# Performance work log

Measured on AMD Instinct MI355X. Metric: run time of the kernel, lower is better.

The kernel has to match this reference:

```python
import jax, jax.numpy as jnp
import numpy as np

NUM_NODES = 2048
NUM_REL = 8
HIDDEN = 256


def setup_inputs() -> dict:
    key = jax.random.key(0)
    k1, k2, k3 = jax.random.split(key, 3)
    X = jax.random.normal(k1, (NUM_NODES, HIDDEN, NUM_REL), dtype=jnp.float32)
    A = jax.random.uniform(k2, (NUM_NODES, NUM_NODES, NUM_REL), dtype=jnp.float32)
    # nn.init.normal_(std=0.01)
    weight = 0.01 * jax.random.normal(k3, (HIDDEN, HIDDEN, NUM_REL), dtype=jnp.float32)
    return {"X": X, "A": A, "weight": weight}


def _tensor_product(A, B):
    # Faithful to the original: FFT along last (relation) dim, take REAL part of
    # both transformed operands, per-slice matmul, then real part of ifft.
    Af = jnp.real(jnp.fft.fft(A, axis=-1))  # (n1, n2, k)
    Bf = jnp.real(jnp.fft.fft(B, axis=-1))  # (n2, n4, k)
    C = jnp.einsum('nmk,mhk->nhk', Af, Bf)  # batched real matmul over slices k
    return jnp.real(jnp.fft.ifft(C, axis=-1)).astype(A.dtype)


def reference(X, A, weight):
    res = _tensor_product(A, X)          # (num_nodes, hidden, num_rel)
    res = _tensor_product(res, weight)   # (num_nodes, hidden, num_rel)
    return res
```

## Files before the change

kernel.cpp:

```cpp
#include <hip/hip_runtime.h>


typedef __bf16 bf16_t;
typedef __bf16 bf16x2 __attribute__((ext_vector_type(2)));
typedef __bf16 bf16x8 __attribute__((ext_vector_type(8)));
typedef float f32x4 __attribute__((ext_vector_type(4)));

#define R2C 0.70710678118654752f

__device__ __forceinline__ size_t swz(int r, int c, int K) {
  return (size_t)r * K + (c & ~63) + ((((c >> 3) & 7) ^ (r & 7)) << 3) + (c & 7);
}

__device__ __forceinline__ void async_cp16(const void* g, void* l) {
  __builtin_amdgcn_global_load_lds((const __attribute__((address_space(1))) char*)g,
                                   (__attribute__((address_space(3))) char*)l,
                                   16, 0, 0);
}

__device__ __forceinline__ void fwd5(const float x[8], float F[5]) {
  float s04 = x[0] + x[4], d04 = x[0] - x[4];
  float s26 = x[2] + x[6];
  float s15 = x[1] + x[5], s37 = x[3] + x[7];
  float t = (x[1] + x[7]) - (x[3] + x[5]);
  float e = s04 + s26, o = s15 + s37;
  F[0] = e + o;
  F[1] = d04 + R2C * t;
  F[2] = s04 - s26;
  F[3] = d04 - R2C * t;
  F[4] = e - o;
}

__global__ __launch_bounds__(256) void k_pre(const float* __restrict__ X,
                                             const float* __restrict__ A,
                                             const float* __restrict__ W,
                                             bf16_t* __restrict__ Xft,
                                             bf16_t* __restrict__ Af,
                                             bf16_t* __restrict__ Wft) {
  __shared__ bf16_t tx[40][256];
  int b = blockIdx.x;
  if (b < 8192) {
    size_t t = (size_t)b * 256 + threadIdx.x;
    size_t idx = t * 2;
    int n = (int)(idx >> 11), m = (int)(idx & 2047);
    const float4* p = (const float4*)(A + idx * 8);
    float4 q0 = p[0], q1 = p[1], q2 = p[2], q3 = p[3];
    float x0[8] = {q0.x, q0.y, q0.z, q0.w, q1.x, q1.y, q1.z, q1.w};
    float x1[8] = {q2.x, q2.y, q2.z, q2.w, q3.x, q3.y, q3.z, q3.w};
    float F0[5], F1[5];
    fwd5(x0, F0);
    fwd5(x1, F1);
    size_t pos = swz(n, m, 2048);
#pragma unroll
    for (int j = 0; j < 5; j++) {
      bf16x2 v = {(bf16_t)F0[j], (bf16_t)F1[j]};
      *(bf16x2*)(Af + (size_t)j * 4194304 + pos) = v;
    }
  } else if (b < 8448) {
    int bx = b - 8192;
    int m0 = (bx & 7) * 256, h0 = (bx >> 3) * 8;
    int t = threadIdx.x;
    const float4* p = (const float4*)(X + (((size_t)(m0 + t) * 256) + h0) * 8);
#pragma unroll
    for (int h = 0; h < 8; h++) {
      float4 a = p[2 * h], bb = p[2 * h + 1];
      float x[8] = {a.x, a.y, a.z, a.w, bb.x, bb.y, bb.z, bb.w};
      float F[5];
      fwd5(x, F);
#pragma unroll
      for (int j = 0; j < 5; j++) tx[j * 8 + h][t] = (bf16_t)F[j];
    }
    __syncthreads();
#pragma unroll
    for (int it = 0; it < 5; it++) {
      int slot = it * 256 + t;
      int row = slot >> 5, ch = slot & 31;
      int j = row >> 3, hl = row & 7;
      int h = h0 + hl;
      size_t gpos = (size_t)j * 524288 + (size_t)h * 2048 + m0 +
                    ((ch & ~7) << 3) + (((ch & 7) ^ (h & 7)) << 3);
      *(uint4*)(Xft + gpos) = *(const uint4*)(&tx[row][ch * 8]);
    }
  } else {
    int h = b - 8448;
    int hp = threadIdx.x;
    const float4* p = (const float4*)(W + ((size_t)hp * 256 + h) * 8);
    float4 a = p[0], bb = p[1];
    float x[8] = {a.x, a.y, a.z, a.w, bb.x, bb.y, bb.z, bb.w};
    float F[5];
    fwd5(x, F);
    const float sc[5] = {0.125f, 0.25f, 0.25f, 0.25f, 0.125f};
    size_t pos = swz(h, hp, 256);
#pragma unroll
    for (int j = 0; j < 5; j++)
      Wft[(size_t)j * 65536 + pos] = (bf16_t)(F[j] * sc[j]);
  }
}

__global__ __launch_bounds__(256) void gemm_ring(const bf16_t* __restrict__ A,
                                                 const bf16_t* __restrict__ B,
                                                 bf16_t* __restrict__ C, int K,
                                                 size_t ap, size_t bp, size_t cp) {
  __shared__ bf16_t sm[65536];
  const int j = blockIdx.z;
  const bf16_t* Aj = A + (size_t)j * ap;
  const bf16_t* Bj = B + (size_t)j * bp;
  bf16_t* Cj = C + (size_t)j * cp;
  const int n0 = blockIdx.x * 128, h0 = blockIdx.y * 128;
  const int tid = threadIdx.x;
  const int wv = tid >> 6, ln = tid & 63;
  const int quad = ln >> 4, l16 = ln & 15;
  const int wn = (wv & 1) * 64, wh = (wv >> 1) * 64;

  const bf16_t* ga[4];
  const bf16_t* gb[4];
  int lo[4];
#pragma unroll
  for (int s = 0; s < 4; s++) {
    int slot = s * 256 + tid;
    int row = slot >> 3, c16 = slot & 7;
    ga[s] = Aj + (size_t)(n0 + row) * K + c16 * 8;
    gb[s] = Bj + (size_t)(h0 + row) * K + c16 * 8;
    lo[s] = (s * 256 + wv * 64) * 8;
  }

  const int T = K >> 6;
#pragma unroll
  for (int i = 0; i < 3; i++) {
#pragma unroll
    for (int s = 0; s < 4; s++) {
      async_cp16(ga[s] + i * 64, sm + i * 8192 + lo[s]);
      async_cp16(gb[s] + i * 64, sm + 32768 + i * 8192 + lo[s]);
    }
  }

  f32x4 acc[4][4] = {};
  for (int t = 0; t < T; t++) {
    int b = t & 3;
    if (t + 3 < T) {
      int nb = (t + 3) & 3;
#pragma unroll
      for (int s = 0; s < 4; s++) {
        async_cp16(ga[s] + (t + 3) * 64, sm + nb * 8192 + lo[s]);
        async_cp16(gb[s] + (t + 3) * 64, sm + 32768 + nb * 8192 + lo[s]);
      }
      __builtin_amdgcn_s_waitcnt(0x4F78);
    } else if (t + 2 < T) {
      __builtin_amdgcn_s_waitcnt(0x4F70);
    } else if (t + 1 < T) {
      __builtin_amdgcn_s_waitcnt(0xF78);
    } else {
      __builtin_amdgcn_s_waitcnt(0xF70);
    }
    __builtin_amdgcn_s_barrier();
    const bf16_t* Asp = sm + b * 8192;
    const bf16_t* Bsp = sm + 32768 + b * 8192;
#pragma unroll
    for (int kh = 0; kh < 2; kh++) {
      bf16x8 af[4], bfr[4];
      int c16 = kh * 4 + quad;
#pragma unroll
      for (int i = 0; i < 4; i++) {
        int ra = wn + i * 16 + l16;
        int rb = wh + i * 16 + l16;
        af[i] = *(const bf16x8*)(Asp + ra * 64 + ((c16 ^ (ra & 7)) << 3));
        bfr[i] = *(const bf16x8*)(Bsp + rb * 64 + ((c16 ^ (rb & 7)) << 3));
      }
#pragma unroll
      for (int i = 0; i < 4; i++)
#pragma unroll
        for (int t2 = 0; t2 < 4; t2++)
          acc[i][t2] = __builtin_amdgcn_mfma_f32_16x16x32_bf16(af[i], bfr[t2],
                                                               acc[i][t2], 0, 0, 0);
    }
    __builtin_amdgcn_s_barrier();
  }
#pragma unroll
  for (int i = 0; i < 4; i++) {
#pragma unroll
    for (int t = 0; t < 4; t++) {
      int hc = h0 + wh + t * 16 + l16;
#pragma unroll
      for (int rg = 0; rg < 4; rg++) {
        int nr = n0 + wn + i * 16 + quad * 4 + rg;
        Cj[swz(nr, hc, 256)] = (bf16_t)acc[i][t][rg];
      }
    }
  }
}

__global__ __launch_bounds__(256) void gemm_flat(const bf16_t* __restrict__ A,
                                                 const bf16_t* __restrict__ B,
                                                 float* __restrict__ C) {
  __shared__ bf16_t sm[65536];
  const int j = blockIdx.z;
  const bf16_t* Aj = A + (size_t)j * 524288;
  const bf16_t* Bj = B + (size_t)j * 65536;
  float* Cj = C + (size_t)j * 524288;
  const int n0 = blockIdx.x * 128, h0 = blockIdx.y * 128;
  const int tid = threadIdx.x;
  const int wv = tid >> 6, ln = tid & 63;
  const int quad = ln >> 4, l16 = ln & 15;
  const int wn = (wv & 1) * 64, wh = (wv >> 1) * 64;

#pragma unroll
  for (int s = 0; s < 16; s++) {
    int st = s * 256 + tid;
    int row = st >> 5, c = st & 31;
    int lo = (s * 256 + wv * 64) * 8;
    async_cp16(Aj + (size_t)(n0 + row) * 256 + c * 8, sm + lo);
    async_cp16(Bj + (size_t)(h0 + row) * 256 + c * 8, sm + 32768 + lo);
  }
  __builtin_amdgcn_s_waitcnt(0xF70);
  __builtin_amdgcn_s_barrier();

  f32x4 acc[4][4] = {};
#pragma unroll
  for (int kh = 0; kh < 8; kh++) {
    bf16x8 af[4], bfr[4];
    int c16 = kh * 4 + quad;
    int cb = (c16 & ~7) << 3;
#pragma unroll
    for (int i = 0; i < 4; i++) {
      int ra = wn + i * 16 + l16;
      int rb = wh + i * 16 + l16;
      af[i] = *(const bf16x8*)(sm + ra * 256 + cb + (((c16 & 7) ^ (ra & 7)) << 3));
      bfr[i] = *(const bf16x8*)(sm + 32768 + rb * 256 + cb +
                                (((c16 & 7) ^ (rb & 7)) << 3));
    }
#pragma unroll
    for (int i = 0; i < 4; i++)
#pragma unroll
      for (int t = 0; t < 4; t++)
        acc[i][t] = __builtin_amdgcn_mfma_f32_16x16x32_bf16(af[i], bfr[t],
                                                            acc[i][t], 0, 0, 0);
  }
#pragma unroll
  for (int i = 0; i < 4; i++) {
#pragma unroll
    for (int t = 0; t < 4; t++) {
      int hc = h0 + wh + t * 16 + l16;
#pragma unroll
      for (int rg = 0; rg < 4; rg++) {
        int nr = n0 + wn + i * 16 + quad * 4 + rg;
        Cj[(size_t)nr * 256 + hc] = acc[i][t][rg];
      }
    }
  }
}

__global__ __launch_bounds__(256) void k_combine(const float* __restrict__ C2,
                                                 float* __restrict__ out) {
  size_t idx = (size_t)blockIdx.x * 256 + threadIdx.x;
  float c0 = C2[idx];
  float c1 = C2[524288 + idx];
  float c2 = C2[2 * 524288 + idx];
  float c3 = C2[3 * 524288 + idx];
  float c4 = C2[4 * 524288 + idx];
  float o0 = c0 + c1 + c2 + c3 + c4;
  float o4 = c0 - c1 + c2 - c3 + c4;
  float o2 = c0 - c2 + c4;
  float rt = R2C * (c1 - c3);
  float o1 = c0 + rt - c4;
  float o3 = c0 - rt - c4;
  float4* op = (float4*)(out + idx * 8);
  op[0] = make_float4(o0, o1, o2, o3);
  op[1] = make_float4(o4, o3, o2, o1);
}

extern "C" void kernel_launch(void* const* d_in, const int* in_sizes, int n_in,
                              void* d_out, int out_size, void* d_ws, size_t ws_size,
                              hipStream_t stream) {
  const float* X = (const float*)d_in[0];
  const float* A = (const float*)d_in[1];
  const float* W = (const float*)d_in[2];
  float* out = (float*)d_out;
  char* ws = (char*)d_ws;

  bf16_t* Af  = (bf16_t*)(ws);
  bf16_t* Xft = (bf16_t*)(ws + 41943040);
  bf16_t* Wft = (bf16_t*)(ws + 47185920);
  bf16_t* C1  = (bf16_t*)(ws + 47841280);
  float*  C2  = (float*) (ws + 53084160);

  k_pre<<<dim3(8704), 256, 0, stream>>>(X, A, W, Xft, Af, Wft);
  gemm_ring<<<dim3(16, 2, 5), 256, 0, stream>>>(
      Af, Xft, C1, 2048, (size_t)4194304, (size_t)524288, (size_t)524288);
  gemm_flat<<<dim3(16, 2, 5), 256, 0, stream>>>(C1, Wft, C2);
  k_combine<<<dim3(2048), 256, 0, stream>>>(C2, out);
}
```

Before: 256.8 us.

## Fuse second GEMM with inverse-DFT combine; widen A pre-transform stores

The second GEMM now loops over all five frequency slices inside each block, with the next slice's tiles double-buffered through async LDS loads. Each slice result is accumulated into the five inverse-DFT outputs in registers and written straight to the final output. This removes the fp32 C2 intermediate and the separate combine kernel. The A pre-transform also has each thread process 8 consecutive elements and emit 16-byte bf16x8 stores instead of bf16x2 stores. The cost is more accumulator registers per thread and a smaller 64x64 output tile per block.

```diff
diff --git a/kernel.cpp b/kernel.cpp
--- a/kernel.cpp
+++ b/kernel.cpp
@@ -39,25 +39,29 @@
                                              bf16_t* __restrict__ Wft) {
   __shared__ bf16_t tx[40][256];
   int b = blockIdx.x;
-  if (b < 8192) {
+  if (b < 2048) {
     size_t t = (size_t)b * 256 + threadIdx.x;
-    size_t idx = t * 2;
-    int n = (int)(idx >> 11), m = (int)(idx & 2047);
+    size_t idx = t * 8;
+    int n = (int)(idx >> 11), m0 = (int)(idx & 2047);
     const float4* p = (const float4*)(A + idx * 8);
-    float4 q0 = p[0], q1 = p[1], q2 = p[2], q3 = p[3];
-    float x0[8] = {q0.x, q0.y, q0.z, q0.w, q1.x, q1.y, q1.z, q1.w};
-    float x1[8] = {q2.x, q2.y, q2.z, q2.w, q3.x, q3.y, q3.z, q3.w};
-    float F0[5], F1[5];
-    fwd5(x0, F0);
-    fwd5(x1, F1);
-    size_t pos = swz(n, m, 2048);
+    float F[8][5];
+#pragma unroll
+    for (int u = 0; u < 8; u++) {
+      float4 a = p[2 * u], bq = p[2 * u + 1];
+      float x[8] = {a.x, a.y, a.z, a.w, bq.x, bq.y, bq.z, bq.w};
+      fwd5(x, F[u]);
+    }
+    size_t pos = (size_t)n * 2048 + (m0 & ~63) +
+                 ((((m0 >> 3) & 7) ^ (n & 7)) << 3);
 #pragma unroll
     for (int j = 0; j < 5; j++) {
-      bf16x2 v = {(bf16_t)F0[j], (bf16_t)F1[j]};
-      *(bf16x2*)(Af + (size_t)j * 4194304 + pos) = v;
-    }
-  } else if (b < 8448) {
-    int bx = b - 8192;
+      bf16x8 v;
+#pragma unroll
+      for (int u = 0; u < 8; u++) v[u] = (bf16_t)F[u][j];
+      *(bf16x8*)(Af + (size_t)j * 4194304 + pos) = v;
+    }
+  } else if (b < 2304) {
+    int bx = b - 2048;
     int m0 = (bx & 7) * 256, h0 = (bx >> 3) * 8;
     int t = threadIdx.x;
     const float4* p = (const float4*)(X + (((size_t)(m0 + t) * 256) + h0) * 8);
@@ -82,7 +86,7 @@
       *(uint4*)(Xft + gpos) = *(const uint4*)(&tx[row][ch * 8]);
     }
   } else {
-    int h = b - 8448;
+    int h = b - 2304;
     int hp = threadIdx.x;
     const float4* p = (const float4*)(W + ((size_t)hp * 256 + h) * 8);
     float4 a = p[0], bb = p[1];
@@ -189,83 +193,105 @@
   }
 }
 
-__global__ __launch_bounds__(256) void gemm_flat(const bf16_t* __restrict__ A,
-                                                 const bf16_t* __restrict__ B,
-                                                 float* __restrict__ C) {
+__global__ __launch_bounds__(256) void gemm_fc(const bf16_t* __restrict__ C1,
+                                               const bf16_t* __restrict__ Wf,
+                                               float* __restrict__ out) {
   __shared__ bf16_t sm[65536];
-  const int j = blockIdx.z;
-  const bf16_t* Aj = A + (size_t)j * 524288;
-  const bf16_t* Bj = B + (size_t)j * 65536;
-  float* Cj = C + (size_t)j * 524288;
-  const int n0 = blockIdx.x * 128, h0 = blockIdx.y * 128;
+  const int n0 = blockIdx.x * 64, h0 = blockIdx.y * 64;
   const int tid = threadIdx.x;
   const int wv = tid >> 6, ln = tid & 63;
   const int quad = ln >> 4, l16 = ln & 15;
-  const int wn = (wv & 1) * 64, wh = (wv >> 1) * 64;
-
-#pragma unroll
-  for (int s = 0; s < 16; s++) {
-    int st = s * 256 + tid;
-    int row = st >> 5, c = st & 31;
-    int lo = (s * 256 + wv * 64) * 8;
-    async_cp16(Aj + (size_t)(n0 + row) * 256 + c * 8, sm + lo);
-    async_cp16(Bj + (size_t)(h0 + row) * 256 + c * 8, sm + 32768 + lo);
-  }
-  __builtin_amdgcn_s_waitcnt(0xF70);
-  __builtin_amdgcn_s_barrier();
-
-  f32x4 acc[4][4] = {};
-#pragma unroll
-  for (int kh = 0; kh < 8; kh++) {
-    bf16x8 af[4], bfr[4];
-    int c16 = kh * 4 + quad;
-    int cb = (c16 & ~7) << 3;
-#pragma unroll
-    for (int i = 0; i < 4; i++) {
-      int ra = wn + i * 16 + l16;
-      int rb = wh + i * 16 + l16;
-      af[i] = *(const bf16x8*)(sm + ra * 256 + cb + (((c16 & 7) ^ (ra & 7)) << 3));
-      bfr[i] = *(const bf16x8*)(sm + 32768 + rb * 256 + cb +
-                                (((c16 & 7) ^ (rb & 7)) << 3));
-    }
-#pragma unroll
-    for (int i = 0; i < 4; i++)
-#pragma unroll
-      for (int t = 0; t < 4; t++)
-        acc[i][t] = __builtin_amdgcn_mfma_f32_16x16x32_bf16(af[i], bfr[t],
-                                                            acc[i][t], 0, 0, 0);
-  }
-#pragma unroll
-  for (int i = 0; i < 4; i++) {
-#pragma unroll
-    for (int t = 0; t < 4; t++) {
-      int hc = h0 + wh + t * 16 + l16;
-#pragma unroll
-      for (int rg = 0; rg < 4; rg++) {
-        int nr = n0 + wn + i * 16 + quad * 4 + rg;
-        Cj[(size_t)nr * 256 + hc] = acc[i][t][rg];
-      }
-    }
-  }
-}
-
-__global__ __launch_bounds__(256) void k_combine(const float* __restrict__ C2,
-                                                 float* __restrict__ out) {
-  size_t idx = (size_t)blockIdx.x * 256 + threadIdx.x;
-  float c0 = C2[idx];
-  float c1 = C2[524288 + idx];
-  float c2 = C2[2 * 524288 + idx];
-  float c3 = C2[3 * 524288 + idx];
-  float c4 = C2[4 * 524288 + idx];
-  float o0 = c0 + c1 + c2 + c3 + c4;
-  float o4 = c0 - c1 + c2 - c3 + c4;
-  float o2 = c0 - c2 + c4;
-  float rt = R2C * (c1 - c3);
-  float o1 = c0 + rt - c4;
-  float o3 = c0 - rt - c4;
-  float4* op = (float4*)(out + idx * 8);
-  op[0] = make_float4(o0, o1, o2, o3);
-  op[1] = make_float4(o4, o3, o2, o1);
+  const int wn = (wv & 1) * 32, wh = (wv >> 1) * 32;
+
+  const int srow = (tid >> 5), sc8 = (tid & 31) * 8;
+  const int lbase = wv * 512;
+
+#define STAGE_J(jj)                                                          \
+  {                                                                          \
+    const bf16_t* Aj = C1 + (size_t)(jj)*524288 + (size_t)n0 * 256;          \
+    const bf16_t* Bj = Wf + (size_t)(jj)*65536 + (size_t)h0 * 256;           \
+    bf16_t* da = sm + ((jj)&1) * 32768;                                      \
+    bf16_t* db = da + 16384;                                                 \
+    _Pragma("unroll") for (int s = 0; s < 8; s++) {                          \
+      async_cp16(Aj + (size_t)(s * 8 + srow) * 256 + sc8, da + s * 2048 + lbase); \
+      async_cp16(Bj + (size_t)(s * 8 + srow) * 256 + sc8, db + s * 2048 + lbase); \
+    }                                                                        \
+  }
+
+  const float CKJ[5][5] = {
+      {1.f, 1.f, 1.f, 1.f, 1.f},
+      {1.f, R2C, 0.f, -R2C, -1.f},
+      {1.f, 0.f, -1.f, 0.f, 1.f},
+      {1.f, -R2C, 0.f, R2C, -1.f},
+      {1.f, -1.f, 1.f, -1.f, 1.f}};
+
+  f32x4 outk[5][2][2] = {};
+
+  STAGE_J(0);
+#pragma unroll
+  for (int j = 0; j < 5; j++) {
+    if (j < 4) {
+      STAGE_J(j + 1);
+      __builtin_amdgcn_s_waitcnt(0x4F70);
+    } else {
+      __builtin_amdgcn_s_waitcnt(0xF70);
+    }
+    __builtin_amdgcn_s_barrier();
+    const bf16_t* Ab = sm + (j & 1) * 32768;
+    const bf16_t* Bb = Ab + 16384;
+    f32x4 acc[2][2] = {};
+#pragma unroll
+    for (int kh = 0; kh < 8; kh++) {
+      int c16 = kh * 4 + quad;
+      int cb = (c16 & ~7) << 3;
+      bf16x8 af[2], bfr[2];
+#pragma unroll
+      for (int i = 0; i < 2; i++) {
+        int ra = wn + i * 16 + l16;
+        int rb = wh + i * 16 + l16;
+        af[i] = *(const bf16x8*)(Ab + ra * 256 + cb + (((c16 & 7) ^ (ra & 7)) << 3));
+        bfr[i] = *(const bf16x8*)(Bb + rb * 256 + cb + (((c16 & 7) ^ (rb & 7)) << 3));
+      }
+#pragma unroll
+      for (int i = 0; i < 2; i++)
+#pragma unroll
+        for (int t = 0; t < 2; t++)
+          acc[i][t] = __builtin_amdgcn_mfma_f32_16x16x32_bf16(af[i], bfr[t],
+                                                              acc[i][t], 0, 0, 0);
+    }
+#pragma unroll
+    for (int k = 0; k < 5; k++) {
+      if (CKJ[j][k] != 0.f) {
+#pragma unroll
+        for (int i = 0; i < 2; i++)
+#pragma unroll
+          for (int t = 0; t < 2; t++)
+#pragma unroll
+            for (int rg = 0; rg < 4; rg++)
+              outk[k][i][t][rg] += CKJ[j][k] * acc[i][t][rg];
+      }
+    }
+    __builtin_amdgcn_s_barrier();
+  }
+
+#pragma unroll
+  for (int i = 0; i < 2; i++) {
+#pragma unroll
+    for (int rg = 0; rg < 4; rg++) {
+      int n = n0 + wn + i * 16 + quad * 4 + rg;
+#pragma unroll
+      for (int t = 0; t < 2; t++) {
+        int h = h0 + wh + t * 16 + l16;
+        float c0 = outk[0][i][t][rg], c1 = outk[1][i][t][rg];
+        float c2 = outk[2][i][t][rg], c3 = outk[3][i][t][rg];
+        float c4 = outk[4][i][t][rg];
+        float4* op = (float4*)(out + (size_t)n * 2048 + h * 8);
+        op[0] = make_float4(c0, c1, c2, c3);
+        op[1] = make_float4(c4, c3, c2, c1);
+      }
+    }
+  }
+#undef STAGE_J
 }
 
 extern "C" void kernel_launch(void* const* d_in, const int* in_sizes, int n_in,
@@ -281,11 +307,9 @@
   bf16_t* Xft = (bf16_t*)(ws + 41943040);
   bf16_t* Wft = (bf16_t*)(ws + 47185920);
   bf16_t* C1  = (bf16_t*)(ws + 47841280);
-  float*  C2  = (float*) (ws + 53084160);
-
-  k_pre<<<dim3(8704), 256, 0, stream>>>(X, A, W, Xft, Af, Wft);
+
+  k_pre<<<dim3(2560), 256, 0, stream>>>(X, A, W, Xft, Af, Wft);
   gemm_ring<<<dim3(16, 2, 5), 256, 0, stream>>>(
       Af, Xft, C1, 2048, (size_t)4194304, (size_t)524288, (size_t)524288);
-  gemm_flat<<<dim3(16, 2, 5), 256, 0, stream>>>(C1, Wft, C2);
-  k_combine<<<dim3(2048), 256, 0, stream>>>(C2, out);
-}
+  gemm_fc<<<dim3(32, 4), 256, 0, stream>>>(C1, Wft, out);
+}
```

Measured after the change: 253.8 us. About the same (-1.2%).
